# Performance work log

Hardware: AMD Instinct MI355X
Metric: run time of the kernel (lower is better)

Reference implementation:

```python
import jax, jax.numpy as jnp
import numpy as np

B, N, E, D, H, L = 1024, 64, 1024, 128, 4, 2
C = D // H          # per-head out_channels
K = 5               # options per attribute
LN_EPS = 1e-5


def setup_inputs() -> dict:
    key = jax.random.key(0)
    ks = jax.random.split(key, 22)
    s = 0.05
    inp = {
        'x': jax.random.randint(ks[0], (B, N), 0, K),
        'edge_index': jax.random.randint(ks[1], (2, E), 0, N),
        'edge_attr': jax.random.uniform(ks[2], (E, 1), jnp.float32),
        # tokenizer params
        'attr_emb': jax.random.normal(ks[3], (N, D), jnp.float32) * s,
        'opt_emb': jax.random.normal(ks[4], (N, K, D), jnp.float32) * s,
        'prior': jnp.ones((N, 1), jnp.float32),
        # GATv2 params, stacked over layers
        'Wl': jax.random.normal(ks[5], (L, D, D), jnp.float32) * s,
        'bl': jnp.zeros((L, D), jnp.float32),
        'Wr': jax.random.normal(ks[6], (L, D, D), jnp.float32) * s,
        'br': jnp.zeros((L, D), jnp.float32),
        'We': jax.random.normal(ks[7], (L, 1, D), jnp.float32) * s,
        'att': jax.random.normal(ks[8], (L, H, C), jnp.float32) * s,
        'conv_bias': jnp.zeros((L, D), jnp.float32),
        'ln_g': jnp.ones((L, D), jnp.float32),
        'ln_b': jnp.zeros((L, D), jnp.float32),
        # reliability head
        'W1': jax.random.normal(ks[9], (2 * D, D), jnp.float32) * s,
        'b1': jnp.zeros((D,), jnp.float32),
        'W2': jax.random.normal(ks[10], (D, 1), jnp.float32) * s,
        'b2': jnp.zeros((1,), jnp.float32),
    }
    return inp


def _forward(x, edge_index, edge_attr, attr_emb, opt_emb, prior,
             Wl, bl, Wr, br, We, att, conv_bias, ln_g, ln_b, W1, b1, W2, b2):
    Bb, n = x.shape
    # Tokenizer: token_i = p_i * (E_attr[i] + E_val[i](x_i))
    val = opt_emb[jnp.arange(n)[None, :], x]                 # [B,n,D]
    T0 = (attr_emb[None] + val) * prior[None]                # [B,n,D]

    src, dst = edge_index[0], edge_index[1]
    h = T0
    for l in range(Wl.shape[0]):
        xl = (h @ Wl[l] + bl[l]).reshape(Bb, n, H, C)        # source transform
        xr = (h @ Wr[l] + br[l]).reshape(Bb, n, H, C)        # target transform
        e = (edge_attr @ We[l]).reshape(1, E, H, C)          # edge embedding
        msg = xl[:, src]                                     # [B,E,H,C]
        z = jax.nn.leaky_relu(msg + xr[:, dst] + e, 0.2)
        alpha = jnp.einsum('behc,hc->beh', z, att[l])        # [B,E,H]
        # segment softmax over incoming edges per target node
        mx = jnp.full((Bb, n, H), -jnp.inf, alpha.dtype).at[:, dst].max(alpha)
        ex = jnp.exp(alpha - mx[:, dst])
        den = jnp.zeros((Bb, n, H), alpha.dtype).at[:, dst].add(ex)
        a = ex / den[:, dst]                                 # normalized attention
        out = jnp.zeros((Bb, n, H, C), h.dtype).at[:, dst].add(msg * a[..., None])
        g = out.reshape(Bb, n, D) + conv_bias[l]
        mu = g.mean(-1, keepdims=True)
        var = g.var(-1, keepdims=True)
        g = (g - mu) / jnp.sqrt(var + LN_EPS) * ln_g[l] + ln_b[l]
        g = jax.nn.elu(g)
        h = h + g                                            # residual

    hat_T = jnp.concatenate([T0, h], axis=-1)                # [B,n,2D]
    rel = jax.nn.sigmoid(jax.nn.relu(hat_T @ W1 + b1) @ W2 + b2)[..., 0]  # [B,n]
    rw = rel[..., None]
    f_scale = (h * rw).sum(1) / (rw.sum(1) + 1e-8)           # [B,D]
    return f_scale, rel, hat_T


def reference(x, edge_index, edge_attr, attr_emb, opt_emb, prior,
              Wl, bl, Wr, br, We, att, conv_bias, ln_g, ln_b, W1, b1, W2, b2):
    return _forward(x, edge_index, edge_attr, attr_emb, opt_emb, prior,
                    Wl, bl, Wr, br, We, att, conv_bias, ln_g, ln_b, W1, b1, W2, b2)
```

## Files before the change

### kernel.cpp

```cpp
#include <hip/hip_runtime.h>
#include <hip/hip_bf16.h>

#define Bv 1024
#define Nv 64
#define Ev 1024
#define Dv 128
#define Hv 4
#define Lv 2
#define Kv 5
#define PAD  136
#define PADF 132

typedef __hip_bfloat16 bf16;
typedef __attribute__((ext_vector_type(8))) short bf16x8_t;
typedef __attribute__((ext_vector_type(4))) float f32x4_t;
typedef __attribute__((ext_vector_type(2))) float f32x2_t;

__device__ __forceinline__ float b2f(bf16 v) { return __bfloat162float(v); }
__device__ __forceinline__ bf16  f2b(float v) { return __float2bfloat16(v); }

__device__ bf16 g_pWl[(size_t)Lv * 2 * Dv * Dv];
__device__ bf16 g_pWr[(size_t)Lv * 2 * Dv * Dv];
__device__ bf16 g_pW1[(size_t)2 * 2 * Dv * Dv];
__device__ float g_K[Lv * Hv];
__device__ unsigned int g_etab[Ev];
__device__ int          g_off[Nv + 1];

__device__ __forceinline__ unsigned int pack2v(f32x2_t v) {
    union { bf16 b; unsigned short u; } lo, hi;
    lo.b = f2b(v.x); hi.b = f2b(v.y);
    return (unsigned int)lo.u | ((unsigned int)hi.u << 16);
}
__device__ __forceinline__ f32x2_t unpack2v(unsigned int u) {
    union { unsigned int u; float f; } a, b;
    a.u = u << 16;
    b.u = u & 0xffff0000u;
    return (f32x2_t){a.f, b.f};
}

__device__ __forceinline__ bf16x8_t load8(const bf16* p, int elem) {
    return *(const bf16x8_t*)(p + elem);
}
__device__ __forceinline__ f32x4_t load4f(const float* p, int elem) {
    return *(const f32x4_t*)(p + elem);
}
__device__ __forceinline__ f32x2_t lo2(f32x4_t v) { return (f32x2_t){v.x, v.y}; }
__device__ __forceinline__ f32x2_t hi2(f32x4_t v) { return (f32x2_t){v.z, v.w}; }

__device__ void pack_mat(const float* __restrict__ W, bf16* __restrict__ out,
                         int K, int tid, int nth)
{
    const int total = K * 128;
    for (int e = tid; e < total; e += nth) {
        int f    = e >> 9;
        int rem  = e & 511;
        int lane = rem >> 3;
        int i    = rem & 7;
        int kk   = f >> 3;
        int nt   = f & 7;
        int col  = nt * 16 + (lane & 15);
        int k    = kk * 32 + (lane >> 4) * 8 + i;
        float w  = W[k * 128 + col];
        bf16 hi  = f2b(w);
        out[e]         = hi;
        out[total + e] = f2b(w - b2f(hi));
    }
}

__global__ void prep(const int* __restrict__ edge_index, const float* __restrict__ edge_attr,
                     const float* __restrict__ Wl, const float* __restrict__ Wr,
                     const float* __restrict__ W1, const float* __restrict__ We,
                     const float* __restrict__ att)
{
    const int bid = blockIdx.x;
    if (bid == 0) {
        __shared__ int cnt[Nv];
        int tid = threadIdx.x;
        if (tid < Nv) cnt[tid] = 0;
        __syncthreads();
        for (int e = tid; e < Ev; e += blockDim.x)
            atomicAdd(&cnt[edge_index[Ev + e]], 1);
        __syncthreads();
        if (tid == 0) {
            int s = 0;
            for (int t = 0; t < Nv; ++t) { int c = cnt[t]; g_off[t] = s; cnt[t] = s; s += c; }
            g_off[Nv] = s;
        }
        __syncthreads();
        for (int e = tid; e < Ev; e += blockDim.x) {
            int s = edge_index[e];
            int d = edge_index[Ev + e];
            int pos = atomicAdd(&cnt[d], 1);
            union { bf16 b; unsigned short u; } cv;
            cv.b = f2b(edge_attr[e]);
            g_etab[pos] = (unsigned int)(s | (d << 6)) | ((unsigned int)cv.u << 16);
        }
        return;
    }
    const int nth = (gridDim.x - 1) * 256;
    const int tid = (bid - 1) * 256 + threadIdx.x;
    for (int l = 0; l < Lv; ++l) {
        pack_mat(Wl + (size_t)l * Dv * Dv, g_pWl + (size_t)l * 2 * Dv * Dv, Dv, tid, nth);
        pack_mat(Wr + (size_t)l * Dv * Dv, g_pWr + (size_t)l * 2 * Dv * Dv, Dv, tid, nth);
    }
    pack_mat(W1, g_pW1, 2 * Dv, tid, nth);
    if (bid == 1 && threadIdx.x < Lv * Hv) {
        int l = threadIdx.x / Hv, h = threadIdx.x % Hv;
        float k = 0.f;
        for (int c = 0; c < 32; ++c)
            k += att[l * Dv + h * 32 + c] * We[l * Dv + h * 32 + c];
        g_K[threadIdx.x] = 0.2f * k;
    }
}

__global__ __launch_bounds__(512, 2)
void gat_fused(const int* __restrict__ x,
               const float* __restrict__ attr_emb,
               const float* __restrict__ opt_emb, const float* __restrict__ prior,
               const float* __restrict__ bl, const float* __restrict__ br,
               const float* __restrict__ conv_bias, const float* __restrict__ ln_g,
               const float* __restrict__ ln_b,
               const float* __restrict__ b1, const float* __restrict__ W2,
               const float* __restrict__ b2,
               const float* __restrict__ We, const float* __restrict__ att,
               float* __restrict__ out_fscale, float* __restrict__ out_rel,
               float* __restrict__ out_hatT)
{
    const int b = blockIdx.x;
    const int tid = threadIdx.x;

    __shared__ __align__(16) bf16  hs [Nv * PAD];
    __shared__ __align__(16) bf16  t0b[Nv * PAD];
    __shared__ __align__(16) float xls[Nv * PADF];
    __shared__ __align__(16) float xrs[Nv * PADF];
    __shared__ __align__(16) bf16 alphas[Ev * Hv];
    __shared__ __align__(16) float red [Nv * 8];
    __shared__ __align__(16) float red2[Nv * 8];
    __shared__ __align__(16) float watt[256];
    __shared__ __align__(16) float w2col[Dv];
    __shared__ float relbuf[Nv];

    const int my_t = tid & 63;
    const int beg  = g_off[my_t];
    const int end  = g_off[my_t + 1];

    for (int idx = tid; idx < Nv * Dv; idx += 512) {
        int n = idx >> 7, d = idx & 127;
        float t0 = (attr_emb[n * Dv + d] + opt_emb[(n * Kv + x[b * Nv + n]) * Dv + d])
                   * prior[n];
        hs[n * PAD + d] = f2b(t0);
    }

    for (int l = 0; l < Lv; ++l) {
        if (tid < 256) {
            int h = tid >> 6, cp = (tid >> 2) & 15, e = tid & 3;
            int c = cp * 2 + (e & 1);
            watt[tid] = (e < 2) ? We[l * Dv + h * 32 + c] : att[l * Dv + h * 32 + c];
        }
        __syncthreads();

        {
            const int w = tid >> 6, lane = tid & 63;
            const int row16 = lane & 15, kg = lane >> 4;
            const bf16* pB = (w < 4) ? (g_pWl + (size_t)l * 2 * Dv * Dv)
                                     : (g_pWr + (size_t)l * 2 * Dv * Dv);
            const int wc = (w & 3) * 32;
            float* dst = (w < 4) ? xls : xrs;
            const float* bias = (w < 4) ? (bl + l * Dv) : (br + l * Dv);

            #pragma unroll
            for (int nt = 0; nt < 2; ++nt) {
                f32x4_t acc[4];
                #pragma unroll
                for (int mt = 0; mt < 4; ++mt)
                    acc[mt] = (f32x4_t){0.f, 0.f, 0.f, 0.f};

                #pragma unroll
                for (int kk = 0; kk < 4; ++kk) {
                    const int kb = kk * 32 + kg * 8;
                    const int f = kk * 8 + (w & 3) * 2 + nt;
                    bf16x8_t bh  = *(const bf16x8_t*)&pB[(size_t)(f * 64 + lane) * 8];
                    bf16x8_t blo = *(const bf16x8_t*)&pB[Dv * Dv + (size_t)(f * 64 + lane) * 8];
                    #pragma unroll
                    for (int mt = 0; mt < 4; ++mt) {
                        bf16x8_t a = load8(hs, (mt * 16 + row16) * PAD + kb);
                        acc[mt] = __builtin_amdgcn_mfma_f32_16x16x32_bf16(a, bh,  acc[mt], 0, 0, 0);
                        acc[mt] = __builtin_amdgcn_mfma_f32_16x16x32_bf16(a, blo, acc[mt], 0, 0, 0);
                    }
                }
                const int col = wc + nt * 16 + row16;
                const float bv = bias[col];
                #pragma unroll
                for (int mt = 0; mt < 4; ++mt) {
                    #pragma unroll
                    for (int r = 0; r < 4; ++r) {
                        const int row = mt * 16 + kg * 4 + r;
                        dst[row * PADF + col] = acc[mt][r] + bv;
                    }
                }
            }
        }
        __syncthreads();

        {
            const int t = tid & 63, h = (tid >> 6) & 3, half = tid >> 8;
            const int ch0 = h * 32 + half * 16;
            f32x4_t a0 = load4f(xls, t * PADF + ch0);
            f32x4_t a1 = load4f(xls, t * PADF + ch0 + 4);
            f32x4_t a2 = load4f(xls, t * PADF + ch0 + 8);
            f32x4_t a3 = load4f(xls, t * PADF + ch0 + 12);
            const float* wb = &watt[h * 64 + half * 32];
            f32x2_t dl2 = {0.f, 0.f};
            dl2 += *(const f32x2_t*)(wb + 0*4 + 2) * lo2(a0);
            dl2 += *(const f32x2_t*)(wb + 1*4 + 2) * hi2(a0);
            dl2 += *(const f32x2_t*)(wb + 2*4 + 2) * lo2(a1);
            dl2 += *(const f32x2_t*)(wb + 3*4 + 2) * hi2(a1);
            dl2 += *(const f32x2_t*)(wb + 4*4 + 2) * lo2(a2);
            dl2 += *(const f32x2_t*)(wb + 5*4 + 2) * hi2(a2);
            dl2 += *(const f32x2_t*)(wb + 6*4 + 2) * lo2(a3);
            dl2 += *(const f32x2_t*)(wb + 7*4 + 2) * hi2(a3);
            red[t * 8 + h * 2 + half] = dl2.x + dl2.y;
        }
        __syncthreads();

        {
            const int h = (tid >> 6) & 3, half = tid >> 8, lane = tid & 63;
            const float k02 = g_K[l * Hv + h];
            const f32x2_t zero2 = {0.f, 0.f};
            unsigned int ets[8];
            #pragma unroll
            for (int e = 0; e < 8; ++e)
                ets[e] = g_etab[(half * 8 + e) * 64 + lane];
            f32x2_t acc[8];
            #pragma unroll
            for (int e = 0; e < 8; ++e) acc[e] = (f32x2_t){0.f, 0.f};

            #pragma unroll
            for (int q = 0; q < 4; ++q) {
                f32x4_t wa[4];
                #pragma unroll
                for (int j = 0; j < 4; ++j)
                    wa[j] = *(const f32x4_t*)&watt[h * 64 + (q * 4 + j) * 4];
                #pragma unroll
                for (int e = 0; e < 8; ++e) {
                    int s = ets[e] & 63, t = (ets[e] >> 6) & 63;
                    f32x4_t xl0 = load4f(xls, s * PADF + h * 32 + q * 8);
                    f32x4_t xl1 = load4f(xls, s * PADF + h * 32 + q * 8 + 4);
                    f32x4_t xr0 = load4f(xrs, t * PADF + h * 32 + q * 8);
                    f32x4_t xr1 = load4f(xrs, t * PADF + h * 32 + q * 8 + 4);
                    union { unsigned int u; float f; } ec; ec.u = ets[e] & 0xffff0000u;
                    f32x2_t ea2 = {ec.f, ec.f};
                    f32x2_t v, we2, at2;
                    we2 = (f32x2_t){wa[0].x, wa[0].y}; at2 = (f32x2_t){wa[0].z, wa[0].w};
                    v = lo2(xl0) + lo2(xr0) + ea2 * we2;
                    acc[e] += at2 * __builtin_elementwise_max(v, zero2);
                    we2 = (f32x2_t){wa[1].x, wa[1].y}; at2 = (f32x2_t){wa[1].z, wa[1].w};
                    v = hi2(xl0) + hi2(xr0) + ea2 * we2;
                    acc[e] += at2 * __builtin_elementwise_max(v, zero2);
                    we2 = (f32x2_t){wa[2].x, wa[2].y}; at2 = (f32x2_t){wa[2].z, wa[2].w};
                    v = lo2(xl1) + lo2(xr1) + ea2 * we2;
                    acc[e] += at2 * __builtin_elementwise_max(v, zero2);
                    we2 = (f32x2_t){wa[3].x, wa[3].y}; at2 = (f32x2_t){wa[3].z, wa[3].w};
                    v = hi2(xl1) + hi2(xr1) + ea2 * we2;
                    acc[e] += at2 * __builtin_elementwise_max(v, zero2);
                }
            }
            #pragma unroll
            for (int e = 0; e < 8; ++e) {
                int s = ets[e] & 63;
                union { unsigned int u; float f; } ec; ec.u = ets[e] & 0xffff0000u;
                float dL = red[s * 8 + h * 2] + red[s * 8 + h * 2 + 1];
                float alpha = 0.2f * dL + k02 * ec.f + 0.8f * (acc[e].x + acc[e].y);
                alphas[((half * 8 + e) * 64 + lane) * Hv + h] = f2b(alpha);
            }
        }
        __syncthreads();

        {
            const int t = my_t, h = (tid >> 6) & 3, half = tid >> 8;
            const int ch0 = h * 32 + half * 16;
            float mx = -3e38f;
            for (int idx = beg; idx < end; ++idx)
                mx = fmaxf(mx, b2f(alphas[idx * Hv + h]));
            f32x2_t acc2[8];
            #pragma unroll
            for (int j = 0; j < 8; ++j) acc2[j] = (f32x2_t){0.f, 0.f};
            float den = 0.f;
            for (int idx = beg; idx < end; ++idx) {
                int s = (int)(g_etab[idx] & 63u);
                float ex = expf(b2f(alphas[idx * Hv + h]) - mx);
                den += ex;
                f32x2_t ex2 = {ex, ex};
                f32x4_t m0 = load4f(xls, s * PADF + ch0);
                f32x4_t m1 = load4f(xls, s * PADF + ch0 + 4);
                f32x4_t m2 = load4f(xls, s * PADF + ch0 + 8);
                f32x4_t m3 = load4f(xls, s * PADF + ch0 + 12);
                acc2[0] += ex2 * lo2(m0); acc2[1] += ex2 * hi2(m0);
                acc2[2] += ex2 * lo2(m1); acc2[3] += ex2 * hi2(m1);
                acc2[4] += ex2 * lo2(m2); acc2[5] += ex2 * hi2(m2);
                acc2[6] += ex2 * lo2(m3); acc2[7] += ex2 * hi2(m3);
            }
            float inv_den = (end > beg) ? 1.f / den : 0.f;
            f32x2_t id2 = {inv_den, inv_den};
            f32x2_t sum2 = {0.f, 0.f}, sq2 = {0.f, 0.f};
            #pragma unroll
            for (int j = 0; j < 8; ++j) {
                f32x2_t cb = *(const f32x2_t*)&conv_bias[l * Dv + ch0 + 2 * j];
                f32x2_t g  = acc2[j] * id2 + cb;
                acc2[j] = g;
                sum2 += g; sq2 += g * g;
            }
            red [t * 8 + h * 2 + half] = sum2.x + sum2.y;
            red2[t * 8 + h * 2 + half] = sq2.x + sq2.y;
            __syncthreads();
            float mu = 0.f, ms = 0.f;
            #pragma unroll
            for (int j = 0; j < 8; ++j) { mu += red[t * 8 + j]; ms += red2[t * 8 + j]; }
            mu *= (1.f / 128.f); ms *= (1.f / 128.f);
            float rstd = rsqrtf(ms - mu * mu + 1e-5f);
            f32x2_t mu2 = {mu, mu}, rs2 = {rstd, rstd};
            #pragma unroll
            for (int j = 0; j < 8; ++j) {
                f32x2_t lg = *(const f32x2_t*)&ln_g[l * Dv + ch0 + 2 * j];
                f32x2_t lb = *(const f32x2_t*)&ln_b[l * Dv + ch0 + 2 * j];
                f32x2_t g  = (acc2[j] - mu2) * rs2 * lg + lb;
                g.x = g.x > 0.f ? g.x : (expf(g.x) - 1.f);
                g.y = g.y > 0.f ? g.y : (expf(g.y) - 1.f);
                unsigned int* hp = (unsigned int*)&hs[t * PAD + ch0 + 2 * j];
                f32x2_t hv = unpack2v(*hp) + g;
                *hp = pack2v(hv);
            }
        }
        __syncthreads();
    }

    if (tid < Dv) w2col[tid] = W2[tid];
    for (int idx = tid; idx < Nv * Dv; idx += 512) {
        int n = idx >> 7, d = idx & 127;
        float t0 = (attr_emb[n * Dv + d] + opt_emb[(n * Kv + x[b * Nv + n]) * Dv + d])
                   * prior[n];
        t0b[n * PAD + d] = f2b(t0);
        size_t rb = ((size_t)(b * Nv + n)) * (2 * Dv);
        out_hatT[rb + d]      = t0;
        out_hatT[rb + Dv + d] = b2f(hs[n * PAD + d]);
    }
    __syncthreads();

    {
        const int w = tid >> 6, lane = tid & 63;
        const int row16 = lane & 15, kg = lane >> 4;
        f32x4_t acc[4];
        #pragma unroll
        for (int mt = 0; mt < 4; ++mt)
            acc[mt] = (f32x4_t){0.f, 0.f, 0.f, 0.f};

        #pragma unroll
        for (int kk = 0; kk < 8; ++kk) {
            const bf16* asrc = (kk < 4) ? t0b : hs;
            const int kb = (kk & 3) * 32 + kg * 8;
            const int f = kk * 8 + w;
            bf16x8_t bh  = *(const bf16x8_t*)&g_pW1[(size_t)(f * 64 + lane) * 8];
            bf16x8_t blo = *(const bf16x8_t*)&g_pW1[(size_t)2 * Dv * Dv + (size_t)(f * 64 + lane) * 8];
            #pragma unroll
            for (int mt = 0; mt < 4; ++mt) {
                bf16x8_t a = load8(asrc, (mt * 16 + row16) * PAD + kb);
                acc[mt] = __builtin_amdgcn_mfma_f32_16x16x32_bf16(a, bh,  acc[mt], 0, 0, 0);
                acc[mt] = __builtin_amdgcn_mfma_f32_16x16x32_bf16(a, blo, acc[mt], 0, 0, 0);
            }
        }
        const int col = w * 16 + row16;
        const float bv = b1[col];
        #pragma unroll
        for (int mt = 0; mt < 4; ++mt) {
            #pragma unroll
            for (int r = 0; r < 4; ++r) {
                const int row = mt * 16 + kg * 4 + r;
                float v = acc[mt][r] + bv;
                xls[row * PADF + col] = v > 0.f ? v : 0.f;
            }
        }
    }
    __syncthreads();

    {
        const int t = tid & 63, h = (tid >> 6) & 3, half = tid >> 8;
        const int ch0 = h * 32 + half * 16;
        f32x4_t h0 = load4f(xls, t * PADF + ch0);
        f32x4_t h1 = load4f(xls, t * PADF + ch0 + 4);
        f32x4_t h2 = load4f(xls, t * PADF + ch0 + 8);
        f32x4_t h3 = load4f(xls, t * PADF + ch0 + 12);
        f32x2_t s2 = {0.f, 0.f};
        s2 += lo2(h0) * *(const f32x2_t*)&w2col[ch0 + 0];
        s2 += hi2(h0) * *(const f32x2_t*)&w2col[ch0 + 2];
        s2 += lo2(h1) * *(const f32x2_t*)&w2col[ch0 + 4];
        s2 += hi2(h1) * *(const f32x2_t*)&w2col[ch0 + 6];
        s2 += lo2(h2) * *(const f32x2_t*)&w2col[ch0 + 8];
        s2 += hi2(h2) * *(const f32x2_t*)&w2col[ch0 + 10];
        s2 += lo2(h3) * *(const f32x2_t*)&w2col[ch0 + 12];
        s2 += hi2(h3) * *(const f32x2_t*)&w2col[ch0 + 14];
        red[t * 8 + h * 2 + half] = s2.x + s2.y;
        __syncthreads();
        if (h == 0 && half == 0) {
            float z = b2[0];
            #pragma unroll
            for (int j = 0; j < 8; ++j) z += red[t * 8 + j];
            float r = 1.f / (1.f + expf(-z));
            relbuf[t] = r;
            out_rel[b * Nv + t] = r;
        }
    }
    __syncthreads();

    if (tid < Dv) {
        float num = 0.f, den = 0.f;
        for (int n = 0; n < Nv; ++n) {
            float r = relbuf[n];
            num += b2f(hs[n * PAD + tid]) * r;
            den += r;
        }
        out_fscale[b * Dv + tid] = num / (den + 1e-8f);
    }
}

extern "C" void kernel_launch(void* const* d_in, const int* in_sizes, int n_in,
                              void* d_out, int out_size, void* d_ws, size_t ws_size,
                              hipStream_t stream)
{
    const int*   x          = (const int*)  d_in[0];
    const int*   edge_index = (const int*)  d_in[1];
    const float* edge_attr  = (const float*)d_in[2];
    const float* attr_emb   = (const float*)d_in[3];
    const float* opt_emb    = (const float*)d_in[4];
    const float* prior      = (const float*)d_in[5];
    const float* Wl         = (const float*)d_in[6];
    const float* bl         = (const float*)d_in[7];
    const float* Wr         = (const float*)d_in[8];
    const float* br         = (const float*)d_in[9];
    const float* We         = (const float*)d_in[10];
    const float* att        = (const float*)d_in[11];
    const float* conv_bias  = (const float*)d_in[12];
    const float* ln_g       = (const float*)d_in[13];
    const float* ln_b       = (const float*)d_in[14];
    const float* W1         = (const float*)d_in[15];
    const float* b1         = (const float*)d_in[16];
    const float* W2         = (const float*)d_in[17];
    const float* b2         = (const float*)d_in[18];

    float* out        = (float*)d_out;
    float* out_fscale = out;
    float* out_rel    = out + (size_t)Bv * Dv;
    float* out_hatT   = out + (size_t)Bv * Dv + (size_t)Bv * Nv;

    prep<<<129, 256, 0, stream>>>(edge_index, edge_attr, Wl, Wr, W1, We, att);
    gat_fused<<<Bv, 512, 0, stream>>>(x, attr_emb, opt_emb,
                                      prior, bl, br, conv_bias,
                                      ln_g, ln_b, b1, W2, b2, We, att,
                                      out_fscale, out_rel, out_hatT);
}
```

Measured before the change: 266.4 us.

## Double block size to 1024 threads and split per-thread work across more waves

Launches the fused GAT kernel with 1024 threads per block instead of 512. Each phase is re-partitioned so every thread does half the work: the projection GEMM gives one 16-column tile per wave, edge scoring and aggregation handle 4 edges or 8 channels per thread, and the reliability-head GEMM splits rows across waves. Reduction buffers grow to 16 partial sums per node. The aim is more parallelism per block to hide latency, at the cost of register pressure under launch_bounds(1024,2), more partial-sum reductions, and more waves waiting at each barrier.

Result: slower. 324.3 us (+21.7%).

```diff
diff --git a/kernel.cpp b/kernel.cpp
--- a/kernel.cpp
+++ b/kernel.cpp
@@ -113,7 +113,7 @@
     }
 }
 
-__global__ __launch_bounds__(512, 2)
+__global__ __launch_bounds__(1024, 2)
 void gat_fused(const int* __restrict__ x,
                const float* __restrict__ attr_emb,
                const float* __restrict__ opt_emb, const float* __restrict__ prior,
@@ -134,8 +134,8 @@
     __shared__ __align__(16) float xls[Nv * PADF];
     __shared__ __align__(16) float xrs[Nv * PADF];
     __shared__ __align__(16) bf16 alphas[Ev * Hv];
-    __shared__ __align__(16) float red [Nv * 8];
-    __shared__ __align__(16) float red2[Nv * 8];
+    __shared__ __align__(16) float red [Nv * 16];
+    __shared__ __align__(16) float red2[Nv * 16];
     __shared__ __align__(16) float watt[256];
     __shared__ __align__(16) float w2col[Dv];
     __shared__ float relbuf[Nv];
@@ -144,7 +144,7 @@
     const int beg  = g_off[my_t];
     const int end  = g_off[my_t + 1];
 
-    for (int idx = tid; idx < Nv * Dv; idx += 512) {
+    for (int idx = tid; idx < Nv * Dv; idx += 1024) {
         int n = idx >> 7, d = idx & 127;
         float t0 = (attr_emb[n * Dv + d] + opt_emb[(n * Kv + x[b * Nv + n]) * Dv + d])
                    * prior[n];
@@ -162,78 +162,69 @@
         {
             const int w = tid >> 6, lane = tid & 63;
             const int row16 = lane & 15, kg = lane >> 4;
-            const bf16* pB = (w < 4) ? (g_pWl + (size_t)l * 2 * Dv * Dv)
+            const bf16* pB = (w < 8) ? (g_pWl + (size_t)l * 2 * Dv * Dv)
                                      : (g_pWr + (size_t)l * 2 * Dv * Dv);
-            const int wc = (w & 3) * 32;
-            float* dst = (w < 4) ? xls : xrs;
-            const float* bias = (w < 4) ? (bl + l * Dv) : (br + l * Dv);
-
-            #pragma unroll
-            for (int nt = 0; nt < 2; ++nt) {
-                f32x4_t acc[4];
-                #pragma unroll
-                for (int mt = 0; mt < 4; ++mt)
-                    acc[mt] = (f32x4_t){0.f, 0.f, 0.f, 0.f};
-
-                #pragma unroll
-                for (int kk = 0; kk < 4; ++kk) {
-                    const int kb = kk * 32 + kg * 8;
-                    const int f = kk * 8 + (w & 3) * 2 + nt;
-                    bf16x8_t bh  = *(const bf16x8_t*)&pB[(size_t)(f * 64 + lane) * 8];
-                    bf16x8_t blo = *(const bf16x8_t*)&pB[Dv * Dv + (size_t)(f * 64 + lane) * 8];
-                    #pragma unroll
-                    for (int mt = 0; mt < 4; ++mt) {
-                        bf16x8_t a = load8(hs, (mt * 16 + row16) * PAD + kb);
-                        acc[mt] = __builtin_amdgcn_mfma_f32_16x16x32_bf16(a, bh,  acc[mt], 0, 0, 0);
-                        acc[mt] = __builtin_amdgcn_mfma_f32_16x16x32_bf16(a, blo, acc[mt], 0, 0, 0);
-                    }
-                }
-                const int col = wc + nt * 16 + row16;
-                const float bv = bias[col];
+            const int nt = w & 7;
+            float* dst = (w < 8) ? xls : xrs;
+            const float* bias = (w < 8) ? (bl + l * Dv) : (br + l * Dv);
+
+            f32x4_t acc[4];
+            #pragma unroll
+            for (int mt = 0; mt < 4; ++mt)
+                acc[mt] = (f32x4_t){0.f, 0.f, 0.f, 0.f};
+
+            #pragma unroll
+            for (int kk = 0; kk < 4; ++kk) {
+                const int kb = kk * 32 + kg * 8;
+                const int f = kk * 8 + nt;
+                bf16x8_t bh  = *(const bf16x8_t*)&pB[(size_t)(f * 64 + lane) * 8];
+                bf16x8_t blo = *(const bf16x8_t*)&pB[Dv * Dv + (size_t)(f * 64 + lane) * 8];
                 #pragma unroll
                 for (int mt = 0; mt < 4; ++mt) {
-                    #pragma unroll
-                    for (int r = 0; r < 4; ++r) {
-                        const int row = mt * 16 + kg * 4 + r;
-                        dst[row * PADF + col] = acc[mt][r] + bv;
-                    }
+                    bf16x8_t a = load8(hs, (mt * 16 + row16) * PAD + kb);
+                    acc[mt] = __builtin_amdgcn_mfma_f32_16x16x32_bf16(a, bh,  acc[mt], 0, 0, 0);
+                    acc[mt] = __builtin_amdgcn_mfma_f32_16x16x32_bf16(a, blo, acc[mt], 0, 0, 0);
                 }
             }
+            const int col = nt * 16 + row16;
+            const float bv = bias[col];
+            #pragma unroll
+            for (int mt = 0; mt < 4; ++mt) {
+                #pragma unroll
+                for (int r = 0; r < 4; ++r) {
+                    const int row = mt * 16 + kg * 4 + r;
+                    dst[row * PADF + col] = acc[mt][r] + bv;
+                }
+            }
         }
         __syncthreads();
 
         {
-            const int t = tid & 63, h = (tid >> 6) & 3, half = tid >> 8;
-            const int ch0 = h * 32 + half * 16;
+            const int t = tid & 63, h = (tid >> 6) & 3, q = tid >> 8;
+            const int ch0 = h * 32 + q * 8;
             f32x4_t a0 = load4f(xls, t * PADF + ch0);
             f32x4_t a1 = load4f(xls, t * PADF + ch0 + 4);
-            f32x4_t a2 = load4f(xls, t * PADF + ch0 + 8);
-            f32x4_t a3 = load4f(xls, t * PADF + ch0 + 12);
-            const float* wb = &watt[h * 64 + half * 32];
+            const float* wb = &watt[h * 64 + q * 16];
             f32x2_t dl2 = {0.f, 0.f};
             dl2 += *(const f32x2_t*)(wb + 0*4 + 2) * lo2(a0);
             dl2 += *(const f32x2_t*)(wb + 1*4 + 2) * hi2(a0);
             dl2 += *(const f32x2_t*)(wb + 2*4 + 2) * lo2(a1);
             dl2 += *(const f32x2_t*)(wb + 3*4 + 2) * hi2(a1);
-            dl2 += *(const f32x2_t*)(wb + 4*4 + 2) * lo2(a2);
-            dl2 += *(const f32x2_t*)(wb + 5*4 + 2) * hi2(a2);
-            dl2 += *(const f32x2_t*)(wb + 6*4 + 2) * lo2(a3);
-            dl2 += *(const f32x2_t*)(wb + 7*4 + 2) * hi2(a3);
-            red[t * 8 + h * 2 + half] = dl2.x + dl2.y;
+            red[t * 16 + h * 4 + q] = dl2.x + dl2.y;
         }
         __syncthreads();
 
         {
-            const int h = (tid >> 6) & 3, half = tid >> 8, lane = tid & 63;
+            const int h = (tid >> 6) & 3, qr = tid >> 8, lane = tid & 63;
             const float k02 = g_K[l * Hv + h];
             const f32x2_t zero2 = {0.f, 0.f};
-            unsigned int ets[8];
-            #pragma unroll
-            for (int e = 0; e < 8; ++e)
-                ets[e] = g_etab[(half * 8 + e) * 64 + lane];
-            f32x2_t acc[8];
-            #pragma unroll
-            for (int e = 0; e < 8; ++e) acc[e] = (f32x2_t){0.f, 0.f};
+            unsigned int ets[4];
+            #pragma unroll
+            for (int e = 0; e < 4; ++e)
+                ets[e] = g_etab[(qr * 4 + e) * 64 + lane];
+            f32x2_t acc[4];
+            #pragma unroll
+            for (int e = 0; e < 4; ++e) acc[e] = (f32x2_t){0.f, 0.f};
 
             #pragma unroll
             for (int q = 0; q < 4; ++q) {
@@ -242,7 +233,7 @@
                 for (int j = 0; j < 4; ++j)
                     wa[j] = *(const f32x4_t*)&watt[h * 64 + (q * 4 + j) * 4];
                 #pragma unroll
-                for (int e = 0; e < 8; ++e) {
+                for (int e = 0; e < 4; ++e) {
                     int s = ets[e] & 63, t = (ets[e] >> 6) & 63;
                     f32x4_t xl0 = load4f(xls, s * PADF + h * 32 + q * 8);
                     f32x4_t xl1 = load4f(xls, s * PADF + h * 32 + q * 8 + 4);
@@ -266,25 +257,26 @@
                 }
             }
             #pragma unroll
-            for (int e = 0; e < 8; ++e) {
+            for (int e = 0; e < 4; ++e) {
                 int s = ets[e] & 63;
                 union { unsigned int u; float f; } ec; ec.u = ets[e] & 0xffff0000u;
-                float dL = red[s * 8 + h * 2] + red[s * 8 + h * 2 + 1];
+                float dL = red[s * 16 + h * 4] + red[s * 16 + h * 4 + 1]
+                         + red[s * 16 + h * 4 + 2] + red[s * 16 + h * 4 + 3];
                 float alpha = 0.2f * dL + k02 * ec.f + 0.8f * (acc[e].x + acc[e].y);
-                alphas[((half * 8 + e) * 64 + lane) * Hv + h] = f2b(alpha);
+                alphas[((qr * 4 + e) * 64 + lane) * Hv + h] = f2b(alpha);
             }
         }
         __syncthreads();
 
         {
-            const int t = my_t, h = (tid >> 6) & 3, half = tid >> 8;
-            const int ch0 = h * 32 + half * 16;
+            const int t = my_t, h = (tid >> 6) & 3, q = tid >> 8;
+            const int ch0 = h * 32 + q * 8;
             float mx = -3e38f;
             for (int idx = beg; idx < end; ++idx)
                 mx = fmaxf(mx, b2f(alphas[idx * Hv + h]));
-            f32x2_t acc2[8];
-            #pragma unroll
-            for (int j = 0; j < 8; ++j) acc2[j] = (f32x2_t){0.f, 0.f};
+            f32x2_t acc2[4];
+            #pragma unroll
+            for (int j = 0; j < 4; ++j) acc2[j] = (f32x2_t){0.f, 0.f};
             float den = 0.f;
             for (int idx = beg; idx < end; ++idx) {
                 int s = (int)(g_etab[idx] & 63u);
@@ -293,34 +285,30 @@
                 f32x2_t ex2 = {ex, ex};
                 f32x4_t m0 = load4f(xls, s * PADF + ch0);
                 f32x4_t m1 = load4f(xls, s * PADF + ch0 + 4);
-                f32x4_t m2 = load4f(xls, s * PADF + ch0 + 8);
-                f32x4_t m3 = load4f(xls, s * PADF + ch0 + 12);
                 acc2[0] += ex2 * lo2(m0); acc2[1] += ex2 * hi2(m0);
                 acc2[2] += ex2 * lo2(m1); acc2[3] += ex2 * hi2(m1);
-                acc2[4] += ex2 * lo2(m2); acc2[5] += ex2 * hi2(m2);
-                acc2[6] += ex2 * lo2(m3); acc2[7] += ex2 * hi2(m3);
             }
             float inv_den = (end > beg) ? 1.f / den : 0.f;
             f32x2_t id2 = {inv_den, inv_den};
             f32x2_t sum2 = {0.f, 0.f}, sq2 = {0.f, 0.f};
             #pragma unroll
-            for (int j = 0; j < 8; ++j) {
+            for (int j = 0; j < 4; ++j) {
                 f32x2_t cb = *(const f32x2_t*)&conv_bias[l * Dv + ch0 + 2 * j];
                 f32x2_t g  = acc2[j] * id2 + cb;
                 acc2[j] = g;
                 sum2 += g; sq2 += g * g;
             }
-            red [t * 8 + h * 2 + half] = sum2.x + sum2.y;
-            red2[t * 8 + h * 2 + half] = sq2.x + sq2.y;
+            red [t * 16 + h * 4 + q] = sum2.x + sum2.y;
+            red2[t * 16 + h * 4 + q] = sq2.x + sq2.y;
             __syncthreads();
             float mu = 0.f, ms = 0.f;
             #pragma unroll
-            for (int j = 0; j < 8; ++j) { mu += red[t * 8 + j]; ms += red2[t * 8 + j]; }
+            for (int j = 0; j < 16; ++j) { mu += red[t * 16 + j]; ms += red2[t * 16 + j]; }
             mu *= (1.f / 128.f); ms *= (1.f / 128.f);
             float rstd = rsqrtf(ms - mu * mu + 1e-5f);
             f32x2_t mu2 = {mu, mu}, rs2 = {rstd, rstd};
             #pragma unroll
-            for (int j = 0; j < 8; ++j) {
+            for (int j = 0; j < 4; ++j) {
                 f32x2_t lg = *(const f32x2_t*)&ln_g[l * Dv + ch0 + 2 * j];
                 f32x2_t lb = *(const f32x2_t*)&ln_b[l * Dv + ch0 + 2 * j];
                 f32x2_t g  = (acc2[j] - mu2) * rs2 * lg + lb;
@@ -335,7 +323,7 @@
     }
 
     if (tid < Dv) w2col[tid] = W2[tid];
-    for (int idx = tid; idx < Nv * Dv; idx += 512) {
+    for (int idx = tid; idx < Nv * Dv; idx += 1024) {
         int n = idx >> 7, d = idx & 127;
         float t0 = (attr_emb[n * Dv + d] + opt_emb[(n * Kv + x[b * Nv + n]) * Dv + d])
                    * prior[n];
@@ -349,32 +337,33 @@
     {
         const int w = tid >> 6, lane = tid & 63;
         const int row16 = lane & 15, kg = lane >> 4;
-        f32x4_t acc[4];
+        const int mt2 = w >> 3, nt = w & 7;
+        f32x4_t acc[2];
         #pragma unroll
-        for (int mt = 0; mt < 4; ++mt)
+        for (int mt = 0; mt < 2; ++mt)
             acc[mt] = (f32x4_t){0.f, 0.f, 0.f, 0.f};
 
         #pragma unroll
         for (int kk = 0; kk < 8; ++kk) {
             const bf16* asrc = (kk < 4) ? t0b : hs;
             const int kb = (kk & 3) * 32 + kg * 8;
-            const int f = kk * 8 + w;
+            const int f = kk * 8 + nt;
             bf16x8_t bh  = *(const bf16x8_t*)&g_pW1[(size_t)(f * 64 + lane) * 8];
             bf16x8_t blo = *(const bf16x8_t*)&g_pW1[(size_t)2 * Dv * Dv + (size_t)(f * 64 + lane) * 8];
             #pragma unroll
-            for (int mt = 0; mt < 4; ++mt) {
-                bf16x8_t a = load8(asrc, (mt * 16 + row16) * PAD + kb);
+            for (int mt = 0; mt < 2; ++mt) {
+                bf16x8_t a = load8(asrc, (mt2 * 32 + mt * 16 + row16) * PAD + kb);
                 acc[mt] = __builtin_amdgcn_mfma_f32_16x16x32_bf16(a, bh,  acc[mt], 0, 0, 0);
                 acc[mt] = __builtin_amdgcn_mfma_f32_16x16x32_bf16(a, blo, acc[mt], 0, 0, 0);
             }
         }
-        const int col = w * 16 + row16;
+        const int col = nt * 16 + row16;
         const float bv = b1[col];
         #pragma unroll
-        for (int mt = 0; mt < 4; ++mt) {
+        for (int mt = 0; mt < 2; ++mt) {
             #pragma unroll
             for (int r = 0; r < 4; ++r) {
-                const int row = mt * 16 + kg * 4 + r;
+                const int row = mt2 * 32 + mt * 16 + kg * 4 + r;
                 float v = acc[mt][r] + bv;
                 xls[row * PADF + col] = v > 0.f ? v : 0.f;
             }
@@ -383,27 +372,21 @@
     __syncthreads();
 
     {
-        const int t = tid & 63, h = (tid >> 6) & 3, half = tid >> 8;
-        const int ch0 = h * 32 + half * 16;
+        const int t = tid & 63, h = (tid >> 6) & 3, q = tid >> 8;
+        const int ch0 = h * 32 + q * 8;
         f32x4_t h0 = load4f(xls, t * PADF + ch0);
         f32x4_t h1 = load4f(xls, t * PADF + ch0 + 4);
-        f32x4_t h2 = load4f(xls, t * PADF + ch0 + 8);
-        f32x4_t h3 = load4f(xls, t * PADF + ch0 + 12);
         f32x2_t s2 = {0.f, 0.f};
         s2 += lo2(h0) * *(const f32x2_t*)&w2col[ch0 + 0];
         s2 += hi2(h0) * *(const f32x2_t*)&w2col[ch0 + 2];
         s2 += lo2(h1) * *(const f32x2_t*)&w2col[ch0 + 4];
         s2 += hi2(h1) * *(const f32x2_t*)&w2col[ch0 + 6];
-        s2 += lo2(h2) * *(const f32x2_t*)&w2col[ch0 + 8];
-        s2 += hi2(h2) * *(const f32x2_t*)&w2col[ch0 + 10];
-        s2 += lo2(h3) * *(const f32x2_t*)&w2col[ch0 + 12];
-        s2 += hi2(h3) * *(const f32x2_t*)&w2col[ch0 + 14];
-        red[t * 8 + h * 2 + half] = s2.x + s2.y;
-        __syncthreads();
-        if (h == 0 && half == 0) {
+        red[t * 16 + h * 4 + q] = s2.x + s2.y;
+        __syncthreads();
+        if (h == 0 && q == 0) {
             float z = b2[0];
             #pragma unroll
-            for (int j = 0; j < 8; ++j) z += red[t * 8 + j];
+            for (int j = 0; j < 16; ++j) z += red[t * 16 + j];
             float r = 1.f / (1.f + expf(-z));
             relbuf[t] = r;
             out_rel[b * Nv + t] = r;
@@ -452,8 +435,8 @@
     float* out_hatT   = out + (size_t)Bv * Dv + (size_t)Bv * Nv;
 
     prep<<<129, 256, 0, stream>>>(edge_index, edge_attr, Wl, Wr, W1, We, att);
-    gat_fused<<<Bv, 512, 0, stream>>>(x, attr_emb, opt_emb,
-                                      prior, bl, br, conv_bias,
-                                      ln_g, ln_b, b1, W2, b2, We, att,
-                                      out_fscale, out_rel, out_hatT);
-}
+    gat_fused<<<Bv, 1024, 0, stream>>>(x, attr_emb, opt_emb,
+                                       prior, bl, br, conv_bias,
+                                       ln_g, ln_b, b1, W2, b2, We, att,
+                                       out_fscale, out_rel, out_hatT);
+}
```
